# Kernel optimization log

Hardware: AMD Instinct MI355X
Metric: run time of the kernel (lower is better)

The kernel has to match this reference:

```python
import jax, jax.numpy as jnp
import numpy as np

H = 16          # num_attention_heads
HD = 64         # attention_head_size
ALPHA = 1.5
BANDWIDTH = 1.0
A_EXP = 0.5     # sinkhorn-like exponent 'a'
DIST_SCALE = float(HD)  # alpha < 2 => scale by head_size
EPS = 1e-12     # F.normalize eps


def setup_inputs() -> dict:
    key = jax.random.key(0)
    ks = jax.random.split(key, 5)
    B, L, D = 2, 1024, 1024
    w_scale = 0.02  # keep distances in a non-degenerate range for the power-law kernel
    x = jax.random.normal(ks[0], (B, L, D), dtype=jnp.float32)
    WQ = jax.random.normal(ks[1], (D, D), dtype=jnp.float32) * w_scale
    WK = jax.random.normal(ks[2], (D, D), dtype=jnp.float32) * w_scale
    WV = jax.random.normal(ks[3], (D, D), dtype=jnp.float32) * w_scale
    WO = jax.random.normal(ks[4], (D, D), dtype=jnp.float32) * w_scale
    z = jnp.zeros((D,), dtype=jnp.float32)
    return {"x": x, "WQ": WQ, "bQ": z, "WK": WK, "bK": z,
            "WV": WV, "bV": z, "WO": WO, "bO": z}


def _heads(t, B, L):
    # [B, L, H*HD] -> [B, H, L, HD]
    return t.reshape(B, L, H, HD).transpose(0, 2, 1, 3)


def reference(x, WQ, bQ, WK, bK, WV, bV, WO, bO):
    B, L, D = x.shape
    q = _heads(x @ WQ + bQ, B, L)   # [B,H,L,HD]
    k = _heads(x @ WK + bK, B, L)
    v = _heads(x @ WV + bV, B, L)

    # torch.cdist(q, k, p=2): pairwise euclidean distance [B,H,L,L]
    q2 = jnp.sum(q * q, axis=-1)                      # [B,H,L]
    k2 = jnp.sum(k * k, axis=-1)                      # [B,H,L]
    qk = jnp.einsum('bhid,bhjd->bhij', q, k)          # [B,H,L,L]
    d2 = q2[..., :, None] + k2[..., None, :] - 2.0 * qk
    g_dist = jnp.sqrt(jnp.maximum(d2, EPS)) / DIST_SCALE

    # alpha < 2: power-law kernel (1 + g/sqrt(bw))^(-(d_intrinsic + alpha))
    attn_score = (1.0 + g_dist / np.sqrt(BANDWIDTH)) ** (-(HD + ALPHA))

    # a > 0: Sinkhorn-style row/col renormalization
    N_R = jnp.sum(attn_score, axis=-1)                # [B,H,L] row sums
    N_C = jnp.sum(attn_score, axis=-2)                # [B,H,L] col sums
    K_tilde = (N_R ** (-A_EXP))[..., :, None] * attn_score * (N_C ** (-A_EXP))[..., None, :]

    # F.normalize(p=1, dim=3); entries are positive so |.| sum == sum
    attention_probs = K_tilde / jnp.maximum(jnp.sum(K_tilde, axis=-1, keepdims=True), EPS)

    out = jnp.einsum('bhij,bhjd->bhid', attention_probs, v)   # [B,H,L,HD]
    out = out.transpose(0, 2, 1, 3).reshape(B, L, H * HD)
    return out @ WO + bO
```

## Files before the change

### kernel.cpp

```cpp
#include <hip/hip_runtime.h>
#include <math.h>


typedef __attribute__((ext_vector_type(8))) short short8;
typedef __attribute__((ext_vector_type(4))) float f32x4;

__device__ inline unsigned short f2bf(float f) {
  unsigned int u = __float_as_uint(f);
  unsigned int r = (u + 0x7FFFu + ((u >> 16) & 1u)) >> 16;
  return (unsigned short)r;
}
__device__ inline float bf2f(unsigned short s) {
  return __uint_as_float(((unsigned int)s) << 16);
}
__device__ inline float score_fn(float dot, float sq) {
  float d2 = fmaxf(fmaf(-2.f, dot, sq), 1e-12f);
  float sd = __builtin_amdgcn_sqrtf(d2);
  float lg = __builtin_amdgcn_logf(fmaf(sd, 0.015625f, 1.0f));
  return __builtin_amdgcn_exp2f(-65.5f * lg);
}
__device__ inline unsigned int cvtpk(float lo, float hi) {
  unsigned int r;
  asm("v_cvt_pk_bf16_f32 %0, %1, %2" : "=v"(r) : "v"(lo), "v"(hi));
  return r;
}
#define GLD16(lptr, gptr)                                                      \
  __builtin_amdgcn_global_load_lds(                                            \
      (const __attribute__((address_space(1))) void*)(gptr),                   \
      (__attribute__((address_space(3))) void*)(lptr), 16, 0, 0)

__global__ __launch_bounds__(256) void cvt_f32_bf16(const float* __restrict__ in,
                                                    unsigned short* __restrict__ out) {
  int i = blockIdx.x * 256 + threadIdx.x;
  float4 v = ((const float4*)in)[i];
  out[4 * i + 0] = f2bf(v.x);
  out[4 * i + 1] = f2bf(v.y);
  out[4 * i + 2] = f2bf(v.z);
  out[4 * i + 3] = f2bf(v.w);
}

__global__ __launch_bounds__(256) void wtrans4(const float* __restrict__ W0,
                                               const float* __restrict__ W1,
                                               const float* __restrict__ W2,
                                               const float* __restrict__ W3,
                                               unsigned short* __restrict__ T0,
                                               unsigned short* __restrict__ T1,
                                               unsigned short* __restrict__ T2,
                                               unsigned short* __restrict__ T3) {
  int z = blockIdx.z;
  const float* W = z == 0 ? W0 : z == 1 ? W1 : z == 2 ? W2 : W3;
  unsigned short* WT = z == 0 ? T0 : z == 1 ? T1 : z == 2 ? T2 : T3;
  __shared__ float T[32][33];
  int k0 = blockIdx.x * 32, n0 = blockIdx.y * 32;
  int c = threadIdx.x & 31, r8 = threadIdx.x >> 5;
#pragma unroll
  for (int it = 0; it < 4; ++it) {
    int rr = r8 + it * 8;
    T[rr][c] = W[(size_t)(k0 + rr) * 1024 + n0 + c];
  }
  __syncthreads();
#pragma unroll
  for (int it = 0; it < 4; ++it) {
    int rr = r8 + it * 8;
    WT[(size_t)(n0 + rr) * 1024 + k0 + c] = f2bf(T[c][rr]);
  }
}

__global__ __launch_bounds__(512, 2) void gemm128k64(const unsigned short* __restrict__ A,
                                                     const unsigned short* __restrict__ B0,
                                                     const unsigned short* __restrict__ B1,
                                                     const unsigned short* __restrict__ B2,
                                                     const float* __restrict__ c0,
                                                     const float* __restrict__ c1,
                                                     const float* __restrict__ c2,
                                                     void* __restrict__ Y0,
                                                     void* __restrict__ Y1,
                                                     void* __restrict__ Y2,
                                                     int m0, int m1, int m2) {
  int z = blockIdx.z;
  const unsigned short* BT = z == 0 ? B0 : z == 1 ? B1 : B2;
  const float* bias = z == 0 ? c0 : z == 1 ? c1 : c2;
  void* Y = z == 0 ? Y0 : z == 1 ? Y1 : Y2;
  int mode = z == 0 ? m0 : z == 1 ? m1 : m2;

  __shared__ __align__(16) unsigned short As[2][128 * 64];
  __shared__ __align__(16) unsigned short Bs[2][128 * 64];
  int tid = threadIdx.x;
  int w = tid >> 6, l = tid & 63, g = l >> 4, l15 = l & 15;
  int wm = w >> 2, wn = w & 3;
  int bm = blockIdx.x * 128, bn = blockIdx.y * 128;
  const int x7 = l15 & 7;

  const int i0 = tid, i1 = tid + 512;
  const int r0 = i0 >> 3, s0 = (i0 & 7) ^ (r0 & 7);
  const int r1 = i1 >> 3, s1 = (i1 & 7) ^ (r1 & 7);

  GLD16(&As[0][i0 * 8], &A[(size_t)(bm + r0) * 1024 + s0 * 8]);
  GLD16(&As[0][i1 * 8], &A[(size_t)(bm + r1) * 1024 + s1 * 8]);
  GLD16(&Bs[0][i0 * 8], &BT[(size_t)(bn + r0) * 1024 + s0 * 8]);
  GLD16(&Bs[0][i1 * 8], &BT[(size_t)(bn + r1) * 1024 + s1 * 8]);

  f32x4 acc[4][2];
#pragma unroll
  for (int mi = 0; mi < 4; ++mi)
#pragma unroll
    for (int ni = 0; ni < 2; ++ni)
#pragma unroll
      for (int r = 0; r < 4; ++r) acc[mi][ni][r] = 0.f;

  __syncthreads();
  for (int t = 0; t < 16; ++t) {
    int cur = t & 1;
    if (t < 15) {
      int kn = (t + 1) * 64;
      GLD16(&As[cur ^ 1][i0 * 8], &A[(size_t)(bm + r0) * 1024 + kn + s0 * 8]);
      GLD16(&As[cur ^ 1][i1 * 8], &A[(size_t)(bm + r1) * 1024 + kn + s1 * 8]);
      GLD16(&Bs[cur ^ 1][i0 * 8], &BT[(size_t)(bn + r0) * 1024 + kn + s0 * 8]);
      GLD16(&Bs[cur ^ 1][i1 * 8], &BT[(size_t)(bn + r1) * 1024 + kn + s1 * 8]);
    }
#pragma unroll
    for (int kc = 0; kc < 2; ++kc) {
      const int cread = (((kc << 2) + g) ^ x7) * 8;
      short8 a[4], b[2];
#pragma unroll
      for (int mi = 0; mi < 4; ++mi)
        a[mi] = *(const short8*)&As[cur][(wm * 64 + mi * 16 + l15) * 64 + cread];
#pragma unroll
      for (int ni = 0; ni < 2; ++ni)
        b[ni] = *(const short8*)&Bs[cur][(wn * 32 + ni * 16 + l15) * 64 + cread];
#pragma unroll
      for (int mi = 0; mi < 4; ++mi)
#pragma unroll
        for (int ni = 0; ni < 2; ++ni)
          acc[mi][ni] = __builtin_amdgcn_mfma_f32_16x16x32_bf16(a[mi], b[ni], acc[mi][ni], 0, 0, 0);
    }
    __syncthreads();
  }

#pragma unroll
  for (int ni = 0; ni < 2; ++ni) {
    int n = bn + wn * 32 + ni * 16 + l15;
    float bv = bias[n];
#pragma unroll
    for (int mi = 0; mi < 4; ++mi) {
#pragma unroll
      for (int r = 0; r < 4; ++r) {
        int m = bm + wm * 64 + mi * 16 + 4 * g + r;
        float v = acc[mi][ni][r] + bv;
        if (mode == 0) {
          int b = m >> 10, ll = m & 1023, h = n >> 6, hd = n & 63;
          ((unsigned short*)Y)[(((size_t)(b * 16 + h) * 1024) + ll) * 64 + hd] = f2bf(v);
        } else if (mode == 1) {
          int b = m >> 10, ll = m & 1023, h = n >> 6, hd = n & 63;
          int jp = (ll & ~31) | (((ll >> 2) & 3) * 8 + ((ll >> 4) & 1) * 4 + (ll & 3));
          ((unsigned short*)Y)[(((size_t)(b * 16 + h) * 64) + hd) * 1024 + jp] = f2bf(v);
        } else {
          ((float*)Y)[(size_t)m * 1024 + n] = v;
        }
      }
    }
  }
}

__global__ __launch_bounds__(256) void gemm_st(const unsigned short* __restrict__ A,
                                               const unsigned short* __restrict__ B0,
                                               const unsigned short* __restrict__ B1,
                                               const unsigned short* __restrict__ B2,
                                               const float* __restrict__ c0,
                                               const float* __restrict__ c1,
                                               const float* __restrict__ c2,
                                               void* __restrict__ Y0,
                                               void* __restrict__ Y1,
                                               void* __restrict__ Y2,
                                               int m0, int m1, int m2) {
  int z = blockIdx.z;
  const unsigned short* BT = z == 0 ? B0 : z == 1 ? B1 : B2;
  const float* bias = z == 0 ? c0 : z == 1 ? c1 : c2;
  void* Y = z == 0 ? Y0 : z == 1 ? Y1 : Y2;
  int mode = z == 0 ? m0 : z == 1 ? m1 : m2;

  __shared__ __align__(16) unsigned short As[2][64 * 64];
  __shared__ __align__(16) unsigned short Bs[2][64 * 64];
  int tid = threadIdx.x;
  int w = tid >> 6, l = tid & 63, g = l >> 4, l15 = l & 15;
  int bm = blockIdx.x * 64, bn = blockIdx.y * 64;
  const int arow = w * 16 + l15;
  const int x7 = l15 & 7;

  const int i0s = tid, i1s = 256 + tid;
  const int r0 = i0s >> 3, s0 = (i0s & 7) ^ (r0 & 7);
  const int r1 = i1s >> 3, s1 = (i1s & 7) ^ (r1 & 7);

  GLD16(&As[0][i0s * 8], &A[(size_t)(bm + r0) * 1024 + s0 * 8]);
  GLD16(&As[0][i1s * 8], &A[(size_t)(bm + r1) * 1024 + s1 * 8]);
  GLD16(&Bs[0][i0s * 8], &BT[(size_t)(bn + r0) * 1024 + s0 * 8]);
  GLD16(&Bs[0][i1s * 8], &BT[(size_t)(bn + r1) * 1024 + s1 * 8]);

  f32x4 acc[4];
#pragma unroll
  for (int t = 0; t < 4; ++t)
#pragma unroll
    for (int r = 0; r < 4; ++r) acc[t][r] = 0.f;

  __syncthreads();
  for (int t = 0; t < 16; ++t) {
    int cur = t & 1;
    if (t < 15) {
      int kn = (t + 1) * 64;
      GLD16(&As[cur ^ 1][i0s * 8], &A[(size_t)(bm + r0) * 1024 + kn + s0 * 8]);
      GLD16(&As[cur ^ 1][i1s * 8], &A[(size_t)(bm + r1) * 1024 + kn + s1 * 8]);
      GLD16(&Bs[cur ^ 1][i0s * 8], &BT[(size_t)(bn + r0) * 1024 + kn + s0 * 8]);
      GLD16(&Bs[cur ^ 1][i1s * 8], &BT[(size_t)(bn + r1) * 1024 + kn + s1 * 8]);
    }
#pragma unroll
    for (int kc = 0; kc < 2; ++kc) {
      short8 a = *(const short8*)&As[cur][arow * 64 + ((kc * 4 + g) ^ x7) * 8];
#pragma unroll
      for (int tt = 0; tt < 4; ++tt) {
        short8 b = *(const short8*)&Bs[cur][(tt * 16 + l15) * 64 + ((kc * 4 + g) ^ x7) * 8];
        acc[tt] = __builtin_amdgcn_mfma_f32_16x16x32_bf16(a, b, acc[tt], 0, 0, 0);
      }
    }
    __syncthreads();
  }

#pragma unroll
  for (int t = 0; t < 4; ++t) {
    int n = bn + 16 * t + l15;
    float bv = bias[n];
#pragma unroll
    for (int r = 0; r < 4; ++r) {
      int m = bm + w * 16 + 4 * g + r;
      float v = acc[t][r] + bv;
      if (mode == 0) {
        int b = m >> 10, ll = m & 1023, h = n >> 6, hd = n & 63;
        ((unsigned short*)Y)[(((size_t)(b * 16 + h) * 1024) + ll) * 64 + hd] = f2bf(v);
      } else if (mode == 1) {
        int b = m >> 10, ll = m & 1023, h = n >> 6, hd = n & 63;
        int jp = (ll & ~31) | (((ll >> 2) & 3) * 8 + ((ll >> 4) & 1) * 4 + (ll & 3));
        ((unsigned short*)Y)[(((size_t)(b * 16 + h) * 64) + hd) * 1024 + jp] = f2bf(v);
      } else {
        ((float*)Y)[(size_t)m * 1024 + n] = v;
      }
    }
  }
}

__global__ __launch_bounds__(256) void sqnorm(const unsigned short* __restrict__ Qb,
                                              const unsigned short* __restrict__ Kb,
                                              float* __restrict__ q2,
                                              float* __restrict__ k2) {
  int row = blockIdx.x * 256 + threadIdx.x;
  const unsigned short* src = blockIdx.y ? Kb : Qb;
  float* dst = blockIdx.y ? k2 : q2;
  const short8* p = (const short8*)&src[(size_t)row * 64];
  float s = 0.f;
#pragma unroll
  for (int c = 0; c < 8; ++c) {
    short8 v = p[c];
#pragma unroll
    for (int e = 0; e < 8; ++e) {
      float f = bf2f((unsigned short)v[e]);
      s = fmaf(f, f, s);
    }
  }
  dst[row] = s;
}

__global__ __launch_bounds__(256) void colsum_mfma(const unsigned short* __restrict__ Qb,
                                                   const unsigned short* __restrict__ Kb,
                                                   const float* __restrict__ q2,
                                                   const float* __restrict__ k2,
                                                   float* __restrict__ rnc) {
  __shared__ __align__(16) unsigned short Qd[2][64 * 64];
  __shared__ __align__(16) float q2s[1024];
  int bh = blockIdx.x, jt = blockIdx.y;
  int tid = threadIdx.x, w = tid >> 6, l = tid & 63;
  int g = l >> 4, l15 = l & 15;
  const int x7 = l15 & 7;
  const unsigned short* Qp = Qb + (size_t)bh * 65536;
  const unsigned short* Kp = Kb + (size_t)bh * 65536;
  int j = jt * 64 + w * 16 + l15;

  const int i0s = tid, i1s = 256 + tid;
  const int r0 = i0s >> 3, s0 = (i0s & 7) ^ (r0 & 7);
  const int r1 = i1s >> 3, s1 = (i1s & 7) ^ (r1 & 7);

  GLD16(&q2s[tid * 4], q2 + (size_t)bh * 1024 + tid * 4);
  GLD16(&Qd[0][i0s * 8], Qp + (size_t)r0 * 64 + s0 * 8);
  GLD16(&Qd[0][i1s * 8], Qp + (size_t)r1 * 64 + s1 * 8);

  short8 bk0 = *(const short8*)&Kp[(size_t)j * 64 + 8 * g];
  short8 bk1 = *(const short8*)&Kp[(size_t)j * 64 + 32 + 8 * g];
  float k2j = k2[(size_t)bh * 1024 + j];
  float colacc = 0.f;

  __syncthreads();
  for (int t = 0; t < 16; ++t) {
    int cur = t & 1;
    if (t < 15) {
      int inx = (t + 1) * 64;
      GLD16(&Qd[cur ^ 1][i0s * 8], Qp + (size_t)(inx + r0) * 64 + s0 * 8);
      GLD16(&Qd[cur ^ 1][i1s * 8], Qp + (size_t)(inx + r1) * 64 + s1 * 8);
    }
    const unsigned short* Ql = Qd[cur];
#pragma unroll
    for (int tp = 0; tp < 4; ++tp) {
      int rowb = (16 * tp + l15) * 64;
      short8 a0 = *(const short8*)&Ql[rowb + ((g) ^ x7) * 8];
      short8 a1 = *(const short8*)&Ql[rowb + ((4 + g) ^ x7) * 8];
      f32x4 cf;
#pragma unroll
      for (int r = 0; r < 4; ++r) cf[r] = 0.f;
      cf = __builtin_amdgcn_mfma_f32_16x16x32_bf16(a0, bk0, cf, 0, 0, 0);
      cf = __builtin_amdgcn_mfma_f32_16x16x32_bf16(a1, bk1, cf, 0, 0, 0);
      float4 qv = *(const float4*)&q2s[t * 64 + 16 * tp + 4 * g];
      colacc += score_fn(cf[0], qv.x + k2j);
      colacc += score_fn(cf[1], qv.y + k2j);
      colacc += score_fn(cf[2], qv.z + k2j);
      colacc += score_fn(cf[3], qv.w + k2j);
    }
    __syncthreads();
  }
  colacc += __shfl_xor(colacc, 16);
  colacc += __shfl_xor(colacc, 32);
  if (l < 16) rnc[(size_t)bh * 1024 + jt * 64 + w * 16 + l] = __builtin_amdgcn_rsqf(colacc);
}

__global__ __launch_bounds__(256) void attn_mfma(const unsigned short* __restrict__ Qb,
                                                 const unsigned short* __restrict__ Kb,
                                                 const unsigned short* __restrict__ VTp,
                                                 const float* __restrict__ q2,
                                                 const float* __restrict__ k2,
                                                 const float* __restrict__ rnc,
                                                 unsigned short* __restrict__ AO) {
  __shared__ __align__(16) unsigned short Kd[2][64 * 64];
  __shared__ __align__(16) unsigned short Vd[2][64 * 64];
  __shared__ __align__(16) float k2s[1024];
  __shared__ __align__(16) float rns[1024];
  int bh = blockIdx.x;
  int tid = threadIdx.x, w = tid >> 6, l = tid & 63;
  int g = l >> 4, l15 = l & 15;
  const int x7 = l15 & 7;
  int it0 = blockIdx.y * 64 + w * 16;
  const unsigned short* Qp = Qb + (size_t)bh * 65536;
  const unsigned short* Kp = Kb + (size_t)bh * 65536;
  const unsigned short* Vp = VTp + (size_t)bh * 65536;
  int b = bh >> 4, h = bh & 15;

  const int i0s = tid, i1s = 256 + tid;
  const int r0 = i0s >> 3, s0 = (i0s & 7) ^ (r0 & 7);
  const int r1 = i1s >> 3, s1 = (i1s & 7) ^ (r1 & 7);

  GLD16(&k2s[tid * 4], k2 + (size_t)bh * 1024 + tid * 4);
  GLD16(&rns[tid * 4], rnc + (size_t)bh * 1024 + tid * 4);
  GLD16(&Kd[0][i0s * 8], Kp + (size_t)r0 * 64 + s0 * 8);
  GLD16(&Kd[0][i1s * 8], Kp + (size_t)r1 * 64 + s1 * 8);
  GLD16(&Vd[0][i0s * 8], Vp + (size_t)r0 * 1024 + s0 * 8);
  GLD16(&Vd[0][i1s * 8], Vp + (size_t)r1 * 1024 + s1 * 8);

  short8 bq0 = *(const short8*)&Qp[(size_t)(it0 + l15) * 64 + 8 * g];
  short8 bq1 = *(const short8*)&Qp[(size_t)(it0 + l15) * 64 + 32 + 8 * g];
  float q2l = q2[(size_t)bh * 1024 + it0 + l15];

  f32x4 o[4];
#pragma unroll
  for (int t = 0; t < 4; ++t)
#pragma unroll
    for (int r = 0; r < 4; ++r) o[t][r] = 0.f;
  float dacc = 0.f;

  __syncthreads();
  for (int t = 0; t < 16; ++t) {
    int cur = t & 1;
    if (t < 15) {
      int j0n = (t + 1) * 64;
      GLD16(&Kd[cur ^ 1][i0s * 8], Kp + (size_t)(j0n + r0) * 64 + s0 * 8);
      GLD16(&Kd[cur ^ 1][i1s * 8], Kp + (size_t)(j0n + r1) * 64 + s1 * 8);
      GLD16(&Vd[cur ^ 1][i0s * 8], Vp + (size_t)r0 * 1024 + j0n + s0 * 8);
      GLD16(&Vd[cur ^ 1][i1s * 8], Vp + (size_t)r1 * 1024 + j0n + s1 * 8);
    }
    const unsigned short* Kl = Kd[cur];
    const unsigned short* Vl = Vd[cur];
    int j0 = t * 64;
    float sc[16];
#pragma unroll
    for (int tp = 0; tp < 4; ++tp) {
      int rowb = (16 * tp + l15) * 64;
      short8 a0 = *(const short8*)&Kl[rowb + ((g) ^ x7) * 8];
      short8 a1 = *(const short8*)&Kl[rowb + ((4 + g) ^ x7) * 8];
      f32x4 cf;
#pragma unroll
      for (int r = 0; r < 4; ++r) cf[r] = 0.f;
      cf = __builtin_amdgcn_mfma_f32_16x16x32_bf16(a0, bq0, cf, 0, 0, 0);
      cf = __builtin_amdgcn_mfma_f32_16x16x32_bf16(a1, bq1, cf, 0, 0, 0);
      float4 kv = *(const float4*)&k2s[j0 + 16 * tp + 4 * g];
      float4 rv = *(const float4*)&rns[j0 + 16 * tp + 4 * g];
      sc[tp * 4 + 0] = score_fn(cf[0], q2l + kv.x) * rv.x;
      sc[tp * 4 + 1] = score_fn(cf[1], q2l + kv.y) * rv.y;
      sc[tp * 4 + 2] = score_fn(cf[2], q2l + kv.z) * rv.z;
      sc[tp * 4 + 3] = score_fn(cf[3], q2l + kv.w) * rv.w;
    }
#pragma unroll
    for (int i = 0; i < 16; ++i) dacc += sc[i];
    int pi0[4], pi1[4];
    pi0[0] = (int)cvtpk(sc[0], sc[1]);
    pi0[1] = (int)cvtpk(sc[2], sc[3]);
    pi0[2] = (int)cvtpk(sc[4], sc[5]);
    pi0[3] = (int)cvtpk(sc[6], sc[7]);
    pi1[0] = (int)cvtpk(sc[8], sc[9]);
    pi1[1] = (int)cvtpk(sc[10], sc[11]);
    pi1[2] = (int)cvtpk(sc[12], sc[13]);
    pi1[3] = (int)cvtpk(sc[14], sc[15]);
    short8 pa0 = *(short8*)pi0;
    short8 pa1 = *(short8*)pi1;
#pragma unroll
    for (int tt = 0; tt < 4; ++tt) {
      int rowb = (16 * tt + l15) * 64;
      short8 v0 = *(const short8*)&Vl[rowb + ((g) ^ x7) * 8];
      short8 v1 = *(const short8*)&Vl[rowb + ((4 + g) ^ x7) * 8];
      o[tt] = __builtin_amdgcn_mfma_f32_16x16x32_bf16(pa0, v0, o[tt], 0, 0, 0);
      o[tt] = __builtin_amdgcn_mfma_f32_16x16x32_bf16(pa1, v1, o[tt], 0, 0, 0);
    }
    __syncthreads();
  }

  dacc += __shfl_xor(dacc, 16);
  dacc += __shfl_xor(dacc, 32);
  float dv[4];
#pragma unroll
  for (int r = 0; r < 4; ++r) dv[r] = __shfl(dacc, 4 * g + r);

#pragma unroll
  for (int t = 0; t < 4; ++t) {
#pragma unroll
    for (int r = 0; r < 4; ++r) {
      int m = b * 1024 + it0 + 4 * g + r;
      int n = h * 64 + t * 16 + l15;
      AO[(size_t)m * 1024 + n] = f2bf(o[t][r] / dv[r]);
    }
  }
}

extern "C" void kernel_launch(void* const* d_in, const int* in_sizes, int n_in,
                              void* d_out, int out_size, void* d_ws, size_t ws_size,
                              hipStream_t stream) {
  const float* x  = (const float*)d_in[0];
  const float* WQ = (const float*)d_in[1];
  const float* bQ = (const float*)d_in[2];
  const float* WK = (const float*)d_in[3];
  const float* bK = (const float*)d_in[4];
  const float* WV = (const float*)d_in[5];
  const float* bV = (const float*)d_in[6];
  const float* WO = (const float*)d_in[7];
  const float* bO = (const float*)d_in[8];

  char* base = (char*)d_ws;
  unsigned short* xb  = (unsigned short*)(base);
  unsigned short* WQT = (unsigned short*)(base + (4u  << 20));
  unsigned short* WKT = (unsigned short*)(base + (6u  << 20));
  unsigned short* WVT = (unsigned short*)(base + (8u  << 20));
  unsigned short* WOT = (unsigned short*)(base + (10u << 20));
  unsigned short* Qb  = (unsigned short*)(base + (12u << 20));
  unsigned short* Kb  = (unsigned short*)(base + (16u << 20));
  unsigned short* VTp = (unsigned short*)(base + (20u << 20));
  unsigned short* AOb = (unsigned short*)(base + (24u << 20));
  float* q2  = (float*)(base + (28u << 20));
  float* k2  = (float*)(base + (28u << 20) + (128u << 10));
  float* rnc = (float*)(base + (28u << 20) + (256u << 10));

  cvt_f32_bf16<<<2048, 256, 0, stream>>>(x, xb);
  wtrans4<<<dim3(32, 32, 4), 256, 0, stream>>>(WQ, WK, WV, WO, WQT, WKT, WVT, WOT);

  gemm128k64<<<dim3(16, 8, 3), 512, 0, stream>>>(xb, WQT, WKT, WVT, bQ, bK, bV,
                                                 Qb, Kb, VTp, 0, 0, 1);

  sqnorm<<<dim3(128, 2), 256, 0, stream>>>(Qb, Kb, q2, k2);
  colsum_mfma<<<dim3(32, 16), 256, 0, stream>>>(Qb, Kb, q2, k2, rnc);
  attn_mfma<<<dim3(32, 16), 256, 0, stream>>>(Qb, Kb, VTp, q2, k2, rnc, AOb);

  gemm_st<<<dim3(32, 16, 1), 256, 0, stream>>>(AOb, WOT, WOT, WOT, bO, bO, bO,
                                               d_out, d_out, d_out, 2, 2, 2);
}
```

Before: 109.6 us.

## Materialize score matrix in bf16 to avoid recomputing scores in attention pass

Adds a two-pass path. The first pass computes the power-law scores once, writes them to a bf16 P matrix and accumulates column sums. A small kernel then scales V by the column factor and appends a row of the factors, so the second pass does P·V with MFMA and gets the row normalizer from that extra row. This replaces recomputing the scores in both colsum and attention with about 64MB of extra global traffic. It also changes precision, since row sums now come from bf16 P, and it only runs when the workspace is at least 100MB.

```diff
diff --git a/kernel.cpp b/kernel.cpp
--- a/kernel.cpp
+++ b/kernel.cpp
@@ -265,6 +265,211 @@
     }
   }
   dst[row] = s;
+}
+
+__global__ __launch_bounds__(256, 4) void passA(const unsigned short* __restrict__ Qb,
+                                                const unsigned short* __restrict__ Kb,
+                                                const float* __restrict__ q2,
+                                                const float* __restrict__ k2,
+                                                unsigned short* __restrict__ P,
+                                                float* __restrict__ rnc) {
+  __shared__ __align__(16) unsigned short Qd[2][64 * 64];
+  __shared__ __align__(16) float q2s[1024];
+  __shared__ float colred[4][64];
+  int bh = blockIdx.x, jt = blockIdx.y;
+  int tid = threadIdx.x, w = tid >> 6, l = tid & 63;
+  int g = l >> 4, l15 = l & 15;
+  const int x7 = l15 & 7;
+  const unsigned short* Qp = Qb + (size_t)bh * 65536;
+  const unsigned short* Kp = Kb + (size_t)bh * 65536;
+
+  const int i0s = tid, i1s = 256 + tid;
+  const int r0 = i0s >> 3, s0 = (i0s & 7) ^ (r0 & 7);
+  const int r1 = i1s >> 3, s1 = (i1s & 7) ^ (r1 & 7);
+
+  GLD16(&q2s[tid * 4], q2 + (size_t)bh * 1024 + tid * 4);
+  GLD16(&Qd[0][i0s * 8], Qp + (size_t)r0 * 64 + s0 * 8);
+  GLD16(&Qd[0][i1s * 8], Qp + (size_t)r1 * 64 + s1 * 8);
+
+  short8 ak[4][2];
+#pragma unroll
+  for (int tp = 0; tp < 4; ++tp) {
+#pragma unroll
+    for (int hf = 0; hf < 2; ++hf)
+      ak[tp][hf] = *(const short8*)&Kp[(size_t)(jt * 64 + 16 * tp + l15) * 64 + hf * 32 + 8 * g];
+  }
+  float k2v[16];
+#pragma unroll
+  for (int tp = 0; tp < 4; ++tp) {
+    float4 kk = *(const float4*)&k2[(size_t)bh * 1024 + jt * 64 + 16 * tp + 4 * g];
+    k2v[tp * 4 + 0] = kk.x; k2v[tp * 4 + 1] = kk.y;
+    k2v[tp * 4 + 2] = kk.z; k2v[tp * 4 + 3] = kk.w;
+  }
+  float colpart[16];
+#pragma unroll
+  for (int q = 0; q < 16; ++q) colpart[q] = 0.f;
+
+  __syncthreads();
+  for (int t = 0; t < 16; ++t) {
+    int cur = t & 1;
+    if (t < 15) {
+      int inx = (t + 1) * 64;
+      GLD16(&Qd[cur ^ 1][i0s * 8], Qp + (size_t)(inx + r0) * 64 + s0 * 8);
+      GLD16(&Qd[cur ^ 1][i1s * 8], Qp + (size_t)(inx + r1) * 64 + s1 * 8);
+    }
+    int rowb = (w * 16 + l15) * 64;
+    short8 bq0 = *(const short8*)&Qd[cur][rowb + ((g) ^ x7) * 8];
+    short8 bq1 = *(const short8*)&Qd[cur][rowb + ((4 + g) ^ x7) * 8];
+    float q2l = q2s[t * 64 + w * 16 + l15];
+    int i = t * 64 + w * 16 + l15;
+
+    float sc[16];
+#pragma unroll
+    for (int tp = 0; tp < 4; ++tp) {
+      f32x4 cf;
+#pragma unroll
+      for (int r = 0; r < 4; ++r) cf[r] = 0.f;
+      cf = __builtin_amdgcn_mfma_f32_16x16x32_bf16(ak[tp][0], bq0, cf, 0, 0, 0);
+      cf = __builtin_amdgcn_mfma_f32_16x16x32_bf16(ak[tp][1], bq1, cf, 0, 0, 0);
+#pragma unroll
+      for (int r = 0; r < 4; ++r)
+        sc[tp * 4 + r] = score_fn(cf[r], q2l + k2v[tp * 4 + r]);
+    }
+#pragma unroll
+    for (int q = 0; q < 16; ++q) colpart[q] += sc[q];
+
+    int pi0[4], pi1[4];
+    pi0[0] = (int)cvtpk(sc[0], sc[1]);
+    pi0[1] = (int)cvtpk(sc[2], sc[3]);
+    pi0[2] = (int)cvtpk(sc[4], sc[5]);
+    pi0[3] = (int)cvtpk(sc[6], sc[7]);
+    pi1[0] = (int)cvtpk(sc[8], sc[9]);
+    pi1[1] = (int)cvtpk(sc[10], sc[11]);
+    pi1[2] = (int)cvtpk(sc[12], sc[13]);
+    pi1[3] = (int)cvtpk(sc[14], sc[15]);
+    size_t off = ((size_t)bh * 1024 + i) * 1024 + jt * 64 + 8 * g;
+    *(short8*)&P[off] = *(short8*)pi0;
+    *(short8*)&P[off + 32] = *(short8*)pi1;
+    __syncthreads();
+  }
+
+#pragma unroll
+  for (int q = 0; q < 16; ++q) {
+    float v = colpart[q];
+    v += __shfl_xor(v, 1);
+    v += __shfl_xor(v, 2);
+    v += __shfl_xor(v, 4);
+    v += __shfl_xor(v, 8);
+    colpart[q] = v;
+  }
+  if (l15 == 0) {
+#pragma unroll
+    for (int q = 0; q < 16; ++q)
+      colred[w][16 * (q >> 2) + 4 * g + (q & 3)] = colpart[q];
+  }
+  __syncthreads();
+  if (tid < 64) {
+    float s = colred[0][tid] + colred[1][tid] + colred[2][tid] + colred[3][tid];
+    rnc[(size_t)bh * 1024 + jt * 64 + tid] = __builtin_amdgcn_rsqf(s);
+  }
+}
+
+__global__ __launch_bounds__(256) void vscale(const unsigned short* __restrict__ VTp,
+                                              const float* __restrict__ rnc,
+                                              unsigned short* __restrict__ Vs) {
+  int bh = blockIdx.x, row = blockIdx.y;
+  int j4 = threadIdx.x * 4;
+  unsigned short out[4];
+#pragma unroll
+  for (int e = 0; e < 4; ++e) {
+    int jp = j4 + e;
+    int p = jp & 31;
+    int gg = (p >> 3) & 3, jj = (p >> 2) & 1, rr = p & 3;
+    int jtrue = (jp & ~31) | (16 * jj + 4 * gg + rr);
+    float rv = rnc[(size_t)bh * 1024 + jtrue];
+    if (row < 64) {
+      float v = bf2f(VTp[((size_t)bh * 64 + row) * 1024 + jp]);
+      out[e] = f2bf(v * rv);
+    } else if (row == 64) {
+      out[e] = f2bf(rv);
+    } else {
+      out[e] = 0;
+    }
+  }
+  *(unsigned long long*)&Vs[((size_t)bh * 80 + row) * 1024 + j4] = *(unsigned long long*)out;
+}
+
+__global__ __launch_bounds__(256, 4) void passB(const unsigned short* __restrict__ P,
+                                                const unsigned short* __restrict__ Vs,
+                                                unsigned short* __restrict__ AO) {
+  __shared__ __align__(16) unsigned short Pd[2][64 * 64];
+  __shared__ __align__(16) unsigned short Vd[2][80 * 64];
+  int bh = blockIdx.x, it = blockIdx.y;
+  int tid = threadIdx.x, w = tid >> 6, l = tid & 63;
+  int g = l >> 4, l15 = l & 15;
+  const int x7 = l15 & 7;
+  const unsigned short* Pp = P + (size_t)bh * 1048576;
+  const unsigned short* Vp = Vs + (size_t)bh * 81920;
+  int b = bh >> 4, h = bh & 15;
+
+  const int cP0 = tid, cP1 = tid + 256;
+  const int rP0 = cP0 >> 3, sP0 = (cP0 & 7) ^ (rP0 & 7);
+  const int rP1 = cP1 >> 3, sP1 = (cP1 & 7) ^ (rP1 & 7);
+  const int cV0 = tid, cV1 = tid + 256, cV2 = tid + 512;
+  const int rV0 = cV0 >> 3, sV0 = (cV0 & 7) ^ (rV0 & 7);
+  const int rV1 = cV1 >> 3, sV1 = (cV1 & 7) ^ (rV1 & 7);
+  const int rV2 = cV2 >> 3, sV2 = (cV2 & 7) ^ (rV2 & 7);
+
+  GLD16(&Pd[0][cP0 * 8], Pp + (size_t)(it * 64 + rP0) * 1024 + sP0 * 8);
+  GLD16(&Pd[0][cP1 * 8], Pp + (size_t)(it * 64 + rP1) * 1024 + sP1 * 8);
+  GLD16(&Vd[0][cV0 * 8], Vp + (size_t)rV0 * 1024 + sV0 * 8);
+  GLD16(&Vd[0][cV1 * 8], Vp + (size_t)rV1 * 1024 + sV1 * 8);
+  if (tid < 128) GLD16(&Vd[0][cV2 * 8], Vp + (size_t)rV2 * 1024 + sV2 * 8);
+
+  f32x4 o[5];
+#pragma unroll
+  for (int t5 = 0; t5 < 5; ++t5)
+#pragma unroll
+    for (int r = 0; r < 4; ++r) o[t5][r] = 0.f;
+
+  __syncthreads();
+  for (int t = 0; t < 16; ++t) {
+    int cur = t & 1;
+    if (t < 15) {
+      int jn = (t + 1) * 64;
+      GLD16(&Pd[cur ^ 1][cP0 * 8], Pp + (size_t)(it * 64 + rP0) * 1024 + jn + sP0 * 8);
+      GLD16(&Pd[cur ^ 1][cP1 * 8], Pp + (size_t)(it * 64 + rP1) * 1024 + jn + sP1 * 8);
+      GLD16(&Vd[cur ^ 1][cV0 * 8], Vp + (size_t)rV0 * 1024 + jn + sV0 * 8);
+      GLD16(&Vd[cur ^ 1][cV1 * 8], Vp + (size_t)rV1 * 1024 + jn + sV1 * 8);
+      if (tid < 128) GLD16(&Vd[cur ^ 1][cV2 * 8], Vp + (size_t)rV2 * 1024 + jn + sV2 * 8);
+    }
+    int rowb = (w * 16 + l15) * 64;
+    short8 pa0 = *(const short8*)&Pd[cur][rowb + ((g) ^ x7) * 8];
+    short8 pa1 = *(const short8*)&Pd[cur][rowb + ((4 + g) ^ x7) * 8];
+#pragma unroll
+    for (int t5 = 0; t5 < 5; ++t5) {
+      int vrow = (16 * t5 + l15) * 64;
+      short8 bv0 = *(const short8*)&Vd[cur][vrow + ((g) ^ x7) * 8];
+      short8 bv1 = *(const short8*)&Vd[cur][vrow + ((4 + g) ^ x7) * 8];
+      o[t5] = __builtin_amdgcn_mfma_f32_16x16x32_bf16(pa0, bv0, o[t5], 0, 0, 0);
+      o[t5] = __builtin_amdgcn_mfma_f32_16x16x32_bf16(pa1, bv1, o[t5], 0, 0, 0);
+    }
+    __syncthreads();
+  }
+
+  float dv[4];
+#pragma unroll
+  for (int r = 0; r < 4; ++r) dv[r] = __shfl(o[4][r], 16 * g);
+
+#pragma unroll
+  for (int t5 = 0; t5 < 4; ++t5) {
+#pragma unroll
+    for (int r = 0; r < 4; ++r) {
+      int m = b * 1024 + it * 64 + w * 16 + 4 * g + r;
+      int n = h * 64 + 16 * t5 + l15;
+      AO[(size_t)m * 1024 + n] = f2bf(o[t5][r] / dv[r]);
+    }
+  }
 }
 
 __global__ __launch_bounds__(256) void colsum_mfma(const unsigned short* __restrict__ Qb,
@@ -468,16 +673,24 @@
   float* q2  = (float*)(base + (28u << 20));
   float* k2  = (float*)(base + (28u << 20) + (128u << 10));
   float* rnc = (float*)(base + (28u << 20) + (256u << 10));
+  unsigned short* Vs = (unsigned short*)(base + (30u << 20));
+  unsigned short* P  = (unsigned short*)(base + (36u << 20));
+  const size_t NEEDED = (size_t)100u << 20;
 
   cvt_f32_bf16<<<2048, 256, 0, stream>>>(x, xb);
   wtrans4<<<dim3(32, 32, 4), 256, 0, stream>>>(WQ, WK, WV, WO, WQT, WKT, WVT, WOT);
-
   gemm128k64<<<dim3(16, 8, 3), 512, 0, stream>>>(xb, WQT, WKT, WVT, bQ, bK, bV,
                                                  Qb, Kb, VTp, 0, 0, 1);
-
   sqnorm<<<dim3(128, 2), 256, 0, stream>>>(Qb, Kb, q2, k2);
-  colsum_mfma<<<dim3(32, 16), 256, 0, stream>>>(Qb, Kb, q2, k2, rnc);
-  attn_mfma<<<dim3(32, 16), 256, 0, stream>>>(Qb, Kb, VTp, q2, k2, rnc, AOb);
+
+  if (ws_size >= NEEDED) {
+    passA<<<dim3(32, 16), 256, 0, stream>>>(Qb, Kb, q2, k2, P, rnc);
+    vscale<<<dim3(32, 80), 256, 0, stream>>>(VTp, rnc, Vs);
+    passB<<<dim3(32, 16), 256, 0, stream>>>(P, Vs, AOb);
+  } else {
+    colsum_mfma<<<dim3(32, 16), 256, 0, stream>>>(Qb, Kb, q2, k2, rnc);
+    attn_mfma<<<dim3(32, 16), 256, 0, stream>>>(Qb, Kb, VTp, q2, k2, rnc, AOb);
+  }
 
   gemm_st<<<dim3(32, 16, 1), 256, 0, stream>>>(AOb, WOT, WOT, WOT, bO, bO, bO,
                                                d_out, d_out, d_out, 2, 2, 2);
```

Measured after the change: 109.9 us. No clear change (+0.3%).
